# Performance work log

Measured on AMD Instinct MI355X. Metric: run time of the kernel, lower is better.

Reference implementation:

```python
import jax, jax.numpy as jnp
import numpy as np

B, T, D = 2, 2048, 1024
H = 16
DH = D // H


def setup_inputs() -> dict:
    key = jax.random.key(0)
    ks = jax.random.split(key, 6)
    s = 1.0 / np.sqrt(D)
    return {
        "x": jax.random.normal(ks[0], (B, T, D), dtype=jnp.float32),
        "Wq": jax.random.normal(ks[1], (D, D), dtype=jnp.float32) * s,
        "Wk": jax.random.normal(ks[2], (D, D), dtype=jnp.float32) * s,
        "Wv": jax.random.normal(ks[3], (D, D), dtype=jnp.float32) * s,
        "Wo": jax.random.normal(ks[4], (D, D), dtype=jnp.float32) * s,
        "bo": jax.random.normal(ks[5], (D,), dtype=jnp.float32) * s,
    }


def reference(x, Wq, Wk, Wv, Wo, bo):
    b, t, _ = x.shape
    # separate Q/K/V projections (nn.Linear: x @ W.T, no bias)
    q = (x @ Wq.T).reshape(b, t, H, DH).transpose(0, 2, 1, 3)  # [b,h,t,hd]
    k = (x @ Wk.T).reshape(b, t, H, DH).transpose(0, 2, 1, 3)
    v = (x @ Wv.T).reshape(b, t, H, DH).transpose(0, 2, 1, 3)

    scores = jnp.einsum("bhqd,bhkd->bhqk", q, k)  # [b,h,t,t]
    causal = jnp.triu(jnp.ones((t, t), dtype=bool), k=1)
    scores = jnp.where(causal, -jnp.inf, scores)
    weights = jax.nn.softmax(scores / np.sqrt(DH), axis=-1)
    # dropout p=0.0 -> identity
    ctx = jnp.einsum("bhqk,bhkd->bhqd", weights, v)  # [b,h,t,hd]
    # NOTE: original code reshapes WITHOUT transposing heads back — replicate faithfully
    ctx = ctx.reshape(b, t, H * DH)
    return ctx @ Wo.T + bo
```

## Files before the change

### kernel.cpp

```cpp
#include <hip/hip_runtime.h>
#include <math.h>

#define BATCH 2
#define SEQ   2048
#define DIM   1024
#define NH    16
#define HD    64
#define MTOT  4096

typedef __attribute__((ext_vector_type(8)))  short bf16x8;
typedef __attribute__((ext_vector_type(4)))  float f32x4;
typedef __attribute__((ext_vector_type(16))) float f32x16;
typedef __attribute__((ext_vector_type(2)))  float f32x2;
typedef __attribute__((ext_vector_type(2)))  unsigned u32x2;

__device__ __forceinline__ ushort f2bf(float f) {
    union { float f; unsigned u; } v; v.f = f;
    unsigned r = v.u + 0x7fffu + ((v.u >> 16) & 1u);
    return (ushort)(r >> 16);
}

__device__ __forceinline__ unsigned cvtpk_bf16(float lo, float hi) {
    unsigned r;
    asm("v_cvt_pk_bf16_f32 %0, %1, %2" : "=v"(r) : "v"(lo), "v"(hi));
    return r;
}

__device__ __forceinline__ f32x2 pk_add(f32x2 a, f32x2 b) {
    f32x2 d;
    asm("v_pk_add_f32 %0, %1, %2" : "=v"(d) : "v"(a), "v"(b));
    return d;
}

__device__ __forceinline__ f32x2 pk_mul(f32x2 a, f32x2 b) {
    f32x2 d;
    asm("v_pk_mul_f32 %0, %1, %2" : "=v"(d) : "v"(a), "v"(b));
    return d;
}

__device__ __forceinline__ float fmax3(float a, float b, float c) {
    return fmaxf(fmaxf(a, b), c);
}

__global__ __launch_bounds__(256)
void cast_all(const float* __restrict__ x,
              const float* __restrict__ Wq, const float* __restrict__ Wk,
              const float* __restrict__ Wv, const float* __restrict__ Wo,
              ushort* __restrict__ xb,
              ushort* __restrict__ wqb, ushort* __restrict__ wkb,
              ushort* __restrict__ wvb, ushort* __restrict__ wob)
{
    const int z = blockIdx.y;
    const float* s; ushort* d; int n4;
    if (z == 0)      { s = x;  d = xb;  n4 = MTOT * DIM / 4; }
    else if (z == 1) { s = Wq; d = wqb; n4 = DIM * DIM / 4; }
    else if (z == 2) { s = Wk; d = wkb; n4 = DIM * DIM / 4; }
    else if (z == 3) { s = Wv; d = wvb; n4 = DIM * DIM / 4; }
    else             { s = Wo; d = wob; n4 = DIM * DIM / 4; }
    for (int i = blockIdx.x * blockDim.x + threadIdx.x; i < n4;
         i += gridDim.x * blockDim.x) {
        float4 v = ((const float4*)s)[i];
        ushort4 o;
        o.x = f2bf(v.x); o.y = f2bf(v.y); o.z = f2bf(v.z); o.w = f2bf(v.w);
        ((ushort4*)d)[i] = o;
    }
}

template<int MODE>
__global__ __launch_bounds__(256)
void gemm_bf16(const ushort* __restrict__ A,
               const ushort* __restrict__ W0, const ushort* __restrict__ W1,
               const ushort* __restrict__ W2,
               ushort* __restrict__ D0, ushort* __restrict__ D1,
               ushort* __restrict__ D2,
               const float* __restrict__ bias, float* __restrict__ Fout)
{
    __shared__ __align__(16) ushort As[2][128 * 64];
    __shared__ __align__(16) ushort Bs[2][128 * 64];

    const int tid = threadIdx.x;
    const int w = tid >> 6, l = tid & 63;
    const int g = l >> 4, l15 = l & 15;
    const int wr = w >> 1, wc = w & 1;
    const int brow = blockIdx.x * 128, bcol = blockIdx.y * 128;

    const ushort* W = (MODE == 1) ? W0
                    : (blockIdx.z == 0 ? W0 : (blockIdx.z == 1 ? W1 : W2));
    ushort* Dst = (MODE == 1) ? (ushort*)0
                : (blockIdx.z == 0 ? D0 : (blockIdx.z == 1 ? D1 : D2));

    const int rsub = l >> 3;
    const int gc   = ((l & 7) ^ rsub) * 8;
    const size_t arow0 = (size_t)(brow + 32 * w + rsub) * DIM;
    const size_t brow0 = (size_t)(bcol + 32 * w + rsub) * DIM;

    auto STAGE = [&](int buf, int ktel) {
        #pragma unroll
        for (int i = 0; i < 4; ++i) {
            __builtin_amdgcn_global_load_lds(
                (const __attribute__((address_space(1))) void*)
                    &A[arow0 + (size_t)(8 * i) * DIM + ktel + gc],
                (__attribute__((address_space(3))) void*)
                    &As[buf][(32 * w + 8 * i) * 64], 16, 0, 0);
            __builtin_amdgcn_global_load_lds(
                (const __attribute__((address_space(1))) void*)
                    &W[brow0 + (size_t)(8 * i) * DIM + ktel + gc],
                (__attribute__((address_space(3))) void*)
                    &Bs[buf][(32 * w + 8 * i) * 64], 16, 0, 0);
        }
    };

    STAGE(0, 0);
    STAGE(1, 64);

    f32x4 acc[4][4] = {};

    for (int t = 0; t < 16; ++t) {
        const int cur = t & 1;
        if (t < 15) asm volatile("s_waitcnt vmcnt(8)" ::: "memory");
        else        asm volatile("s_waitcnt vmcnt(0)" ::: "memory");
        __builtin_amdgcn_s_barrier();
        __builtin_amdgcn_sched_barrier(0);

        #pragma unroll
        for (int kh = 0; kh < 2; ++kh) {
            bf16x8 af[4], bfr[4];
            #pragma unroll
            for (int mi = 0; mi < 4; ++mi) {
                int row = 64 * wr + 16 * mi + l15;
                af[mi] = *(const bf16x8*)&As[cur][row * 64 + (((4 * kh + g) ^ (row & 7)) * 8)];
            }
            #pragma unroll
            for (int nj = 0; nj < 4; ++nj) {
                int row = 64 * wc + 16 * nj + l15;
                bfr[nj] = *(const bf16x8*)&Bs[cur][row * 64 + (((4 * kh + g) ^ (row & 7)) * 8)];
            }
            __builtin_amdgcn_s_setprio(1);
            #pragma unroll
            for (int mi = 0; mi < 4; ++mi)
                #pragma unroll
                for (int nj = 0; nj < 4; ++nj)
                    acc[mi][nj] = __builtin_amdgcn_mfma_f32_16x16x32_bf16(
                        af[mi], bfr[nj], acc[mi][nj], 0, 0, 0);
            __builtin_amdgcn_s_setprio(0);
        }

        __builtin_amdgcn_sched_barrier(0);
        __builtin_amdgcn_s_barrier();
        if (t + 2 < 16) STAGE(cur, (t + 2) * 64);
    }

    if (MODE == 0) {
        ushort* LB = (ushort*)As;
        const int bB = brow >> 11, t0 = brow & (SEQ - 1);
        if (blockIdx.z == 2) {
            #pragma unroll
            for (int mi = 0; mi < 4; ++mi)
                #pragma unroll
                for (int nj = 0; nj < 4; ++nj) {
                    int tlb = 64 * wr + 16 * mi + 4 * g;
                    int hd = 16 * nj + l15;
                    int sI = (tlb >> 3) * 2 + wc;
                    uint2 pk;
                    pk.x = cvtpk_bf16(acc[mi][nj][0], acc[mi][nj][1]);
                    pk.y = cvtpk_bf16(acc[mi][nj][2], acc[mi][nj][3]);
                    *(uint2*)&LB[sI * 512 + hd * 8 + (tlb & 7)] = pk;
                }
            __syncthreads();
            #pragma unroll
            for (int j = 0; j < 8; ++j) {
                int4 v = *(const int4*)&LB[(j * 256 + tid) * 8];
                int sI = j * 4 + (tid >> 6);
                size_t base = (size_t)(bB * NH + 2 * blockIdx.y + (sI & 1)) * (SEQ * HD)
                            + (size_t)((t0 >> 3) + (sI >> 1)) * 512 + (tid & 63) * 8;
                *(int4*)&Dst[base] = v;
            }
        } else {
            const float osc = (blockIdx.z == 0) ? 0.125f * 1.44269504f : 1.0f;
            #pragma unroll
            for (int mi = 0; mi < 4; ++mi)
                #pragma unroll
                for (int nj = 0; nj < 4; ++nj)
                    #pragma unroll
                    for (int reg = 0; reg < 4; ++reg) {
                        int tl = 64 * wr + 16 * mi + 4 * g + reg;
                        int hd = 16 * nj + l15;
                        int sI = (tl >> 5) * 2 + wc;
                        LB[sI * 2048 + (hd >> 3) * 256 + (tl & 31) * 8 + (hd & 7)] =
                            f2bf(acc[mi][nj][reg] * osc);
                    }
            __syncthreads();
            #pragma unroll
            for (int j = 0; j < 8; ++j) {
                int4 v = *(const int4*)&LB[(j * 256 + tid) * 8];
                size_t base = (size_t)(bB * NH + 2 * blockIdx.y + (j & 1)) * (SEQ * HD)
                            + (size_t)((t0 >> 5) + (j >> 1)) * 2048 + tid * 8;
                *(int4*)&Dst[base] = v;
            }
        }
    } else {
        #pragma unroll
        for (int nj = 0; nj < 4; ++nj) {
            int col = bcol + 64 * wc + 16 * nj + l15;
            float bv = bias[col];
            #pragma unroll
            for (int mi = 0; mi < 4; ++mi)
                #pragma unroll
                for (int reg = 0; reg < 4; ++reg) {
                    int row = brow + 64 * wr + 16 * mi + 4 * g + reg;
                    Fout[(size_t)row * DIM + col] = acc[mi][nj][reg] + bv;
                }
        }
    }
}

__global__ __launch_bounds__(256, 2)
void attn_mfma9(const ushort* __restrict__ q, const ushort* __restrict__ k,
                const ushort* __restrict__ vt, ushort* __restrict__ ctx)
{
    __shared__ float Olds[4 * 2048];
    __shared__ float Mlds[4][32];
    __shared__ float Llds[4][32];

    const int tid = threadIdx.x;
    const int wq = tid >> 6, l = tid & 63;
    const int l31 = l & 31, h = l >> 5;
    const int bh = blockIdx.x;
    const int qt = 63 - (int)blockIdx.y;
    const int qlo = qt * 32;
    const int nt  = (qt >> 1) + 1;
    const int cnt = (nt + 3) >> 2;
    const int kt0 = wq * cnt;
    const int kt1 = min(nt, kt0 + cnt);

    const ushort* Qg = q  + (size_t)bh * SEQ * HD;
    const ushort* Kg = k  + (size_t)bh * SEQ * HD;
    const ushort* Vg = vt + (size_t)bh * SEQ * HD;

    bf16x8 qf[4];
    #pragma unroll
    for (int s = 0; s < 4; ++s)
        qf[s] = *(const bf16x8*)&Qg[(((size_t)qt * 8 + 2 * s + h) * 32 + l31) * 8];

    f32x16 o[2] = {};
    float m = -3.0e38f, lsum = 0.f;

    if (kt0 < kt1) {
        bf16x8 kfA[8], kfB[8], vfA[8], vfB[8];
        #pragma unroll
        for (int s = 0; s < 4; ++s)
            #pragma unroll
            for (int f = 0; f < 2; ++f)
                kfA[2 * s + f] = *(const bf16x8*)
                    &Kg[(((size_t)(2 * kt0 + f) * 8 + 2 * s + h) * 32 + l31) * 8];
        #pragma unroll
        for (int s4 = 0; s4 < 4; ++s4)
            #pragma unroll
            for (int dt = 0; dt < 2; ++dt)
                vfA[2 * s4 + dt] = *(const bf16x8*)
                    &Vg[(((size_t)(8 * kt0 + 2 * s4 + h)) * 64 + 32 * dt + l31) * 8];

        auto body = [&](bf16x8 (&kc)[8], bf16x8 (&kn)[8],
                        bf16x8 (&vc)[8], bf16x8 (&vn)[8], int kt) {
            const int kvb = 64 * kt;

            f32x16 st[2] = {};
            __builtin_amdgcn_s_setprio(1);
            #pragma unroll
            for (int s = 0; s < 4; ++s)
                #pragma unroll
                for (int f = 0; f < 2; ++f)
                    st[f] = __builtin_amdgcn_mfma_f32_32x32x16_bf16(
                        kc[2 * s + f], qf[s], st[f], 0, 0, 0);
            __builtin_amdgcn_s_setprio(0);

            if (kt + 1 < kt1) {
                #pragma unroll
                for (int s = 0; s < 4; ++s)
                    #pragma unroll
                    for (int f = 0; f < 2; ++f)
                        kn[2 * s + f] = *(const bf16x8*)
                            &Kg[(((size_t)(2 * kt + 2 + f) * 8 + 2 * s + h) * 32 + l31) * 8];
                #pragma unroll
                for (int s4 = 0; s4 < 4; ++s4)
                    #pragma unroll
                    for (int dt = 0; dt < 2; ++dt)
                        vn[2 * s4 + dt] = *(const bf16x8*)
                            &Vg[(((size_t)(8 * kt + 8 + 2 * s4 + h)) * 64 + 32 * dt + l31) * 8];
            }

            const int qg = qlo + l31;
            if (kvb + 63 > qlo) {
                #pragma unroll
                for (int f = 0; f < 2; ++f)
                    #pragma unroll
                    for (int r = 0; r < 16; ++r) {
                        int kvg = kvb + 32 * f + (r & 3) + 8 * (r >> 2) + 4 * h;
                        if (kvg > qg) st[f][r] = -INFINITY;
                    }
            }

            float ca, cb;
            ca = fmax3(st[0][0], st[0][1], st[0][2]);
            cb = fmax3(st[0][3], st[0][4], st[0][5]);
            ca = fmax3(ca, st[0][6], st[0][7]);
            cb = fmax3(cb, st[0][8], st[0][9]);
            ca = fmax3(ca, st[0][10], st[0][11]);
            cb = fmax3(cb, st[0][12], st[0][13]);
            ca = fmax3(ca, st[0][14], st[0][15]);
            float t0 = fmaxf(ca, cb);
            ca = fmax3(st[1][0], st[1][1], st[1][2]);
            cb = fmax3(st[1][3], st[1][4], st[1][5]);
            ca = fmax3(ca, st[1][6], st[1][7]);
            cb = fmax3(cb, st[1][8], st[1][9]);
            ca = fmax3(ca, st[1][10], st[1][11]);
            cb = fmax3(cb, st[1][12], st[1][13]);
            ca = fmax3(ca, st[1][14], st[1][15]);
            float tmax = fmax3(t0, ca, cb);
            {
                union { float f; unsigned u; } tm; tm.f = tmax;
                u32x2 ts = __builtin_amdgcn_permlane32_swap(tm.u, tm.u, false, false);
                union { unsigned u; float f; } to; to.u = h ? ts.x : ts.y;
                tmax = fmaxf(tmax, to.f);
            }

            if (!__all(tmax - m <= 8.0f)) {
                float mn = fmaxf(m, tmax);
                float sc = exp2f(m - mn);
                lsum *= sc;
                f32x2 sc2 = {sc, sc};
                #pragma unroll
                for (int dt = 0; dt < 2; ++dt) {
                    f32x2* po = (f32x2*)&o[dt];
                    #pragma unroll
                    for (int i = 0; i < 8; ++i) po[i] = pk_mul(po[i], sc2);
                }
                m = mn;
            }

            f32x2 mneg = {-m, -m};
            f32x2 a0 = {0.f, 0.f}, a1 = {0.f, 0.f}, a2 = {0.f, 0.f}, a3 = {0.f, 0.f};
            #pragma unroll
            for (int f = 0; f < 2; ++f) {
                f32x2* pp = (f32x2*)&st[f];
                #pragma unroll
                for (int i = 0; i < 8; ++i) {
                    f32x2 t = pk_add(pp[i], mneg);
                    t.x = exp2f(t.x); t.y = exp2f(t.y);
                    pp[i] = t;
                    if ((i & 3) == 0)      a0 = pk_add(a0, t);
                    else if ((i & 3) == 1) a1 = pk_add(a1, t);
                    else if ((i & 3) == 2) a2 = pk_add(a2, t);
                    else                   a3 = pk_add(a3, t);
                }
            }
            a0 = pk_add(a0, a1);
            a2 = pk_add(a2, a3);
            a0 = pk_add(a0, a2);
            lsum += a0.x + a0.y;

            #pragma unroll
            for (int s4 = 0; s4 < 4; ++s4) {
                const int f = s4 >> 1, rb2 = 8 * (s4 & 1);
                unsigned Aa = cvtpk_bf16(st[f][rb2 + 0], st[f][rb2 + 1]);
                unsigned Bb = cvtpk_bf16(st[f][rb2 + 2], st[f][rb2 + 3]);
                unsigned Cc = cvtpk_bf16(st[f][rb2 + 4], st[f][rb2 + 5]);
                unsigned Dd = cvtpk_bf16(st[f][rb2 + 6], st[f][rb2 + 7]);
                u32x2 r02 = __builtin_amdgcn_permlane32_swap(Aa, Cc, false, false);
                u32x2 r13 = __builtin_amdgcn_permlane32_swap(Bb, Dd, false, false);
                union { unsigned wv[4]; bf16x8 v; } pu;
                pu.wv[0] = r02.x;
                pu.wv[1] = r13.x;
                pu.wv[2] = r02.y;
                pu.wv[3] = r13.y;
                __builtin_amdgcn_s_setprio(1);
                #pragma unroll
                for (int dt = 0; dt < 2; ++dt)
                    o[dt] = __builtin_amdgcn_mfma_f32_32x32x16_bf16(
                        vc[2 * s4 + dt], pu.v, o[dt], 0, 0, 0);
                __builtin_amdgcn_s_setprio(0);
            }
        };

        int kt = kt0;
        while (true) {
            body(kfA, kfB, vfA, vfB, kt);
            if (++kt >= kt1) break;
            body(kfB, kfA, vfB, vfA, kt);
            if (++kt >= kt1) break;
        }
    }

    float lt = lsum + __shfl_xor(lsum, 32);
    if (h == 0) Mlds[wq][l31] = m;
    __syncthreads();
    float ms = fmaxf(fmaxf(Mlds[0][l31], Mlds[1][l31]),
                     fmaxf(Mlds[2][l31], Mlds[3][l31]));
    float fw = exp2f(m - ms);
    if (h == 0) Llds[wq][l31] = lt * fw;
    #pragma unroll
    for (int dt = 0; dt < 2; ++dt)
        #pragma unroll
        for (int r = 0; r < 16; ++r) {
            int d = 32 * dt + (r & 3) + 8 * (r >> 2) + 4 * h;
            Olds[wq * 2048 + d * 32 + (l31 ^ (d & 31))] = o[dt][r] * fw;
        }
    __syncthreads();

    const int tq = tid >> 3, tc = tid & 7;
    float inv = 1.0f / (Llds[0][tq] + Llds[1][tq] + Llds[2][tq] + Llds[3][tq]);
    union { ushort u[8]; int4 v4; } ov;
    #pragma unroll
    for (int i = 0; i < 8; i += 2) {
        int d0 = 8 * tc + i, d1 = d0 + 1;
        float s0 = 0.f, s1 = 0.f;
        #pragma unroll
        for (int ww = 0; ww < 4; ++ww) {
            s0 += Olds[ww * 2048 + d0 * 32 + (tq ^ (d0 & 31))];
            s1 += Olds[ww * 2048 + d1 * 32 + (tq ^ (d1 & 31))];
        }
        *(unsigned*)&ov.u[i] = cvtpk_bf16(s0 * inv, s1 * inv);
    }
    ushort* Cg = ctx + (size_t)bh * SEQ * HD + (size_t)qlo * HD;
    *(int4*)&Cg[tq * 64 + 8 * tc] = ov.v4;
}

extern "C" void kernel_launch(void* const* d_in, const int* in_sizes, int n_in,
                              void* d_out, int out_size, void* d_ws, size_t ws_size,
                              hipStream_t stream)
{
    (void)in_sizes; (void)n_in; (void)out_size; (void)ws_size;
    const float* x  = (const float*)d_in[0];
    const float* Wq = (const float*)d_in[1];
    const float* Wk = (const float*)d_in[2];
    const float* Wv = (const float*)d_in[3];
    const float* Wo = (const float*)d_in[4];
    const float* bo = (const float*)d_in[5];
    float* out = (float*)d_out;

    ushort* wsu  = (ushort*)d_ws;
    ushort* xb   = wsu;
    ushort* wqb  = wsu + 4194304;
    ushort* wkb  = wsu + 5242880;
    ushort* wvb  = wsu + 6291456;
    ushort* wob  = wsu + 7340032;
    ushort* qbuf = wsu + 8388608;
    ushort* kbuf = wsu + 12582912;
    ushort* vtb  = wsu + 16777216;
    ushort* ctxb = wsu + 20971520;

    cast_all<<<dim3(512, 5), 256, 0, stream>>>(x, Wq, Wk, Wv, Wo,
                                               xb, wqb, wkb, wvb, wob);

    dim3 gqkv(MTOT / 128, DIM / 128, 3);
    gemm_bf16<0><<<gqkv, 256, 0, stream>>>(xb, wqb, wkb, wvb,
                                           qbuf, kbuf, vtb, nullptr, nullptr);

    dim3 ga(BATCH * NH, SEQ / 32);
    attn_mfma9<<<ga, 256, 0, stream>>>(qbuf, kbuf, vtb, ctxb);

    dim3 go(MTOT / 128, DIM / 128, 1);
    gemm_bf16<1><<<go, 256, 0, stream>>>(ctxb, wob, nullptr, nullptr,
                                         nullptr, nullptr, nullptr, bo, out);
}
```

Before: 106.9 us.

## Software-pipeline QK^T one tile ahead of softmax in attention kernel

Restructures the attention inner loop so the QK^T MFMAs for the next KV tile are issued before the softmax of the current tile, with the K fragments prefetched two tiles ahead. V fragments are now loaded at the start of each iteration instead of being double-buffered a tile ahead. The aim is to overlap the matrix-core work with the exp/max VALU work of the softmax. In exchange it holds a second score accumulator in registers, which raises register pressure, and the V loads have less time to arrive before the PV MFMAs.

```diff
diff --git a/kernel.cpp b/kernel.cpp
--- a/kernel.cpp
+++ b/kernel.cpp
@@ -215,8 +215,8 @@
 }
 
 __global__ __launch_bounds__(256, 2)
-void attn_mfma9(const ushort* __restrict__ q, const ushort* __restrict__ k,
-                const ushort* __restrict__ vt, ushort* __restrict__ ctx)
+void attn_mfma11(const ushort* __restrict__ q, const ushort* __restrict__ k,
+                 const ushort* __restrict__ vt, ushort* __restrict__ ctx)
 {
     __shared__ float Olds[4 * 2048];
     __shared__ float Mlds[4][32];
@@ -246,47 +246,62 @@
     float m = -3.0e38f, lsum = 0.f;
 
     if (kt0 < kt1) {
-        bf16x8 kfA[8], kfB[8], vfA[8], vfB[8];
+        bf16x8 kfA[8], kfB[8];
+        f32x16 stA[2], stB[2];
+
         #pragma unroll
         for (int s = 0; s < 4; ++s)
             #pragma unroll
             for (int f = 0; f < 2; ++f)
                 kfA[2 * s + f] = *(const bf16x8*)
                     &Kg[(((size_t)(2 * kt0 + f) * 8 + 2 * s + h) * 32 + l31) * 8];
-        #pragma unroll
-        for (int s4 = 0; s4 < 4; ++s4)
-            #pragma unroll
-            for (int dt = 0; dt < 2; ++dt)
-                vfA[2 * s4 + dt] = *(const bf16x8*)
-                    &Vg[(((size_t)(8 * kt0 + 2 * s4 + h)) * 64 + 32 * dt + l31) * 8];
-
-        auto body = [&](bf16x8 (&kc)[8], bf16x8 (&kn)[8],
-                        bf16x8 (&vc)[8], bf16x8 (&vn)[8], int kt) {
+        stA[0] = (f32x16){}; stA[1] = (f32x16){};
+        #pragma unroll
+        for (int s = 0; s < 4; ++s)
+            #pragma unroll
+            for (int f = 0; f < 2; ++f)
+                stA[f] = __builtin_amdgcn_mfma_f32_32x32x16_bf16(
+                    kfA[2 * s + f], qf[s], stA[f], 0, 0, 0);
+        if (kt0 + 1 < kt1) {
+            #pragma unroll
+            for (int s = 0; s < 4; ++s)
+                #pragma unroll
+                for (int f = 0; f < 2; ++f)
+                    kfB[2 * s + f] = *(const bf16x8*)
+                        &Kg[(((size_t)(2 * kt0 + 2 + f) * 8 + 2 * s + h) * 32 + l31) * 8];
+        }
+
+        auto body = [&](f32x16 (&stC)[2], f32x16 (&stN)[2],
+                        bf16x8 (&kcN)[8], bf16x8 (&kcL)[8], int kt) {
             const int kvb = 64 * kt;
 
-            f32x16 st[2] = {};
-            __builtin_amdgcn_s_setprio(1);
-            #pragma unroll
-            for (int s = 0; s < 4; ++s)
-                #pragma unroll
-                for (int f = 0; f < 2; ++f)
-                    st[f] = __builtin_amdgcn_mfma_f32_32x32x16_bf16(
-                        kc[2 * s + f], qf[s], st[f], 0, 0, 0);
-            __builtin_amdgcn_s_setprio(0);
+            bf16x8 vf[8];
+            #pragma unroll
+            for (int s4 = 0; s4 < 4; ++s4)
+                #pragma unroll
+                for (int dt = 0; dt < 2; ++dt)
+                    vf[2 * s4 + dt] = *(const bf16x8*)
+                        &Vg[(((size_t)(8 * kt + 2 * s4 + h)) * 64 + 32 * dt + l31) * 8];
 
             if (kt + 1 < kt1) {
+                stN[0] = (f32x16){}; stN[1] = (f32x16){};
+                __builtin_amdgcn_s_setprio(1);
                 #pragma unroll
                 for (int s = 0; s < 4; ++s)
                     #pragma unroll
                     for (int f = 0; f < 2; ++f)
-                        kn[2 * s + f] = *(const bf16x8*)
-                            &Kg[(((size_t)(2 * kt + 2 + f) * 8 + 2 * s + h) * 32 + l31) * 8];
-                #pragma unroll
-                for (int s4 = 0; s4 < 4; ++s4)
+                        stN[f] = __builtin_amdgcn_mfma_f32_32x32x16_bf16(
+                            kcN[2 * s + f], qf[s], stN[f], 0, 0, 0);
+                __builtin_amdgcn_s_setprio(0);
+            }
+
+            if (kt + 2 < kt1) {
+                #pragma unroll
+                for (int s = 0; s < 4; ++s)
                     #pragma unroll
-                    for (int dt = 0; dt < 2; ++dt)
-                        vn[2 * s4 + dt] = *(const bf16x8*)
-                            &Vg[(((size_t)(8 * kt + 8 + 2 * s4 + h)) * 64 + 32 * dt + l31) * 8];
+                    for (int f = 0; f < 2; ++f)
+                        kcL[2 * s + f] = *(const bf16x8*)
+                            &Kg[(((size_t)(2 * kt + 4 + f) * 8 + 2 * s + h) * 32 + l31) * 8];
             }
 
             const int qg = qlo + l31;
@@ -296,26 +311,26 @@
                     #pragma unroll
                     for (int r = 0; r < 16; ++r) {
                         int kvg = kvb + 32 * f + (r & 3) + 8 * (r >> 2) + 4 * h;
-                        if (kvg > qg) st[f][r] = -INFINITY;
+                        if (kvg > qg) stC[f][r] = -INFINITY;
                     }
             }
 
             float ca, cb;
-            ca = fmax3(st[0][0], st[0][1], st[0][2]);
-            cb = fmax3(st[0][3], st[0][4], st[0][5]);
-            ca = fmax3(ca, st[0][6], st[0][7]);
-            cb = fmax3(cb, st[0][8], st[0][9]);
-            ca = fmax3(ca, st[0][10], st[0][11]);
-            cb = fmax3(cb, st[0][12], st[0][13]);
-            ca = fmax3(ca, st[0][14], st[0][15]);
+            ca = fmax3(stC[0][0], stC[0][1], stC[0][2]);
+            cb = fmax3(stC[0][3], stC[0][4], stC[0][5]);
+            ca = fmax3(ca, stC[0][6], stC[0][7]);
+            cb = fmax3(cb, stC[0][8], stC[0][9]);
+            ca = fmax3(ca, stC[0][10], stC[0][11]);
+            cb = fmax3(cb, stC[0][12], stC[0][13]);
+            ca = fmax3(ca, stC[0][14], stC[0][15]);
             float t0 = fmaxf(ca, cb);
-            ca = fmax3(st[1][0], st[1][1], st[1][2]);
-            cb = fmax3(st[1][3], st[1][4], st[1][5]);
-            ca = fmax3(ca, st[1][6], st[1][7]);
-            cb = fmax3(cb, st[1][8], st[1][9]);
-            ca = fmax3(ca, st[1][10], st[1][11]);
-            cb = fmax3(cb, st[1][12], st[1][13]);
-            ca = fmax3(ca, st[1][14], st[1][15]);
+            ca = fmax3(stC[1][0], stC[1][1], stC[1][2]);
+            cb = fmax3(stC[1][3], stC[1][4], stC[1][5]);
+            ca = fmax3(ca, stC[1][6], stC[1][7]);
+            cb = fmax3(cb, stC[1][8], stC[1][9]);
+            ca = fmax3(ca, stC[1][10], stC[1][11]);
+            cb = fmax3(cb, stC[1][12], stC[1][13]);
+            ca = fmax3(ca, stC[1][14], stC[1][15]);
             float tmax = fmax3(t0, ca, cb);
             {
                 union { float f; unsigned u; } tm; tm.f = tmax;
@@ -342,7 +357,7 @@
             f32x2 a0 = {0.f, 0.f}, a1 = {0.f, 0.f}, a2 = {0.f, 0.f}, a3 = {0.f, 0.f};
             #pragma unroll
             for (int f = 0; f < 2; ++f) {
-                f32x2* pp = (f32x2*)&st[f];
+                f32x2* pp = (f32x2*)&stC[f];
                 #pragma unroll
                 for (int i = 0; i < 8; ++i) {
                     f32x2 t = pk_add(pp[i], mneg);
@@ -362,10 +377,10 @@
             #pragma unroll
             for (int s4 = 0; s4 < 4; ++s4) {
                 const int f = s4 >> 1, rb2 = 8 * (s4 & 1);
-                unsigned Aa = cvtpk_bf16(st[f][rb2 + 0], st[f][rb2 + 1]);
-                unsigned Bb = cvtpk_bf16(st[f][rb2 + 2], st[f][rb2 + 3]);
-                unsigned Cc = cvtpk_bf16(st[f][rb2 + 4], st[f][rb2 + 5]);
-                unsigned Dd = cvtpk_bf16(st[f][rb2 + 6], st[f][rb2 + 7]);
+                unsigned Aa = cvtpk_bf16(stC[f][rb2 + 0], stC[f][rb2 + 1]);
+                unsigned Bb = cvtpk_bf16(stC[f][rb2 + 2], stC[f][rb2 + 3]);
+                unsigned Cc = cvtpk_bf16(stC[f][rb2 + 4], stC[f][rb2 + 5]);
+                unsigned Dd = cvtpk_bf16(stC[f][rb2 + 6], stC[f][rb2 + 7]);
                 u32x2 r02 = __builtin_amdgcn_permlane32_swap(Aa, Cc, false, false);
                 u32x2 r13 = __builtin_amdgcn_permlane32_swap(Bb, Dd, false, false);
                 union { unsigned wv[4]; bf16x8 v; } pu;
@@ -377,16 +392,16 @@
                 #pragma unroll
                 for (int dt = 0; dt < 2; ++dt)
                     o[dt] = __builtin_amdgcn_mfma_f32_32x32x16_bf16(
-                        vc[2 * s4 + dt], pu.v, o[dt], 0, 0, 0);
+                        vf[2 * s4 + dt], pu.v, o[dt], 0, 0, 0);
                 __builtin_amdgcn_s_setprio(0);
             }
         };
 
         int kt = kt0;
         while (true) {
-            body(kfA, kfB, vfA, vfB, kt);
+            body(stA, stB, kfB, kfA, kt);
             if (++kt >= kt1) break;
-            body(kfB, kfA, vfB, vfA, kt);
+            body(stB, stA, kfA, kfB, kt);
             if (++kt >= kt1) break;
         }
     }
@@ -457,7 +472,7 @@
                                            qbuf, kbuf, vtb, nullptr, nullptr);
 
     dim3 ga(BATCH * NH, SEQ / 32);
-    attn_mfma9<<<ga, 256, 0, stream>>>(qbuf, kbuf, vtb, ctxb);
+    attn_mfma11<<<ga, 256, 0, stream>>>(qbuf, kbuf, vtb, ctxb);
 
     dim3 go(MTOT / 128, DIM / 128, 1);
     gemm_bf16<1><<<go, 256, 0, stream>>>(ctxb, wob, nullptr, nullptr,
```

Measured after the change: 106.4 us. No clear change (-0.4%).
